# Optimization experiments

Hardware: AMD Instinct MI355X
Metric: run time of the kernel (lower is better)

Reference implementation:

```python
import jax, jax.numpy as jnp
import numpy as np

B, H, T, K, V = 4, 16, 2048, 128, 128


def setup_inputs() -> dict:
    key = jax.random.key(0)
    ks = jax.random.split(key, 5)
    q = jax.random.normal(ks[0], (B, H, T, K), dtype=jnp.float32)
    k = jax.random.normal(ks[1], (B, H, T, K), dtype=jnp.float32)
    v = jax.random.normal(ks[2], (B, H, T, V), dtype=jnp.float32)
    # g is a per-step log decay gate: small negative so exp(g) in (0.95, 1]
    g = -jax.random.uniform(ks[3], (B, H, T), dtype=jnp.float32) * 0.05
    # beta is the delta-rule step size, in (0, 1)
    beta = jax.random.uniform(ks[4], (B, H, T), dtype=jnp.float32)
    initial_state = jnp.zeros((B, H, K, V), dtype=jnp.float32)
    return {"q": q, "k": k, "v": v, "g": g, "beta": beta,
            "initial_state": initial_state}


def _l2norm(x, eps=1e-12):
    # matches F.normalize(p=2, dim=-1): x / max(||x||_2, eps)
    n = jnp.sqrt(jnp.sum(x * x, axis=-1, keepdims=True))
    return x / jnp.maximum(n, eps)


def reference(q, k, v, g, beta, initial_state):
    q = _l2norm(q)
    k = _l2norm(k)
    scale = q.shape[-1] ** -0.5  # default scale of chunk_gated_delta_rule

    # time-major for scan: [T, B, H, ...]
    qT = jnp.moveaxis(q, 2, 0) * scale
    kT = jnp.moveaxis(k, 2, 0)
    vT = jnp.moveaxis(v, 2, 0)
    gT = jnp.moveaxis(g, 2, 0)
    bT = jnp.moveaxis(beta, 2, 0)

    def step(S, inp):
        qt, kt, vt, gt, bt = inp  # qt/kt: [B,H,K], vt: [B,H,V], gt/bt: [B,H]
        S = S * jnp.exp(gt)[..., None, None]           # gated decay of state
        kS = jnp.einsum('bhk,bhkv->bhv', kt, S)        # current prediction
        dv = bt[..., None] * (vt - kS)                 # delta-rule correction
        S = S + jnp.einsum('bhk,bhv->bhkv', kt, dv)    # rank-1 state update
        ot = jnp.einsum('bhk,bhkv->bhv', qt, S)        # readout
        return S, ot

    final_state, oT = jax.lax.scan(step, initial_state, (qT, kT, vT, gT, bT))
    o = jnp.moveaxis(oT, 0, 2)  # [B,H,T,V]
    return o, final_state
```

## Files before the change

kernel.cpp:

```cpp
#include <hip/hip_runtime.h>
#include <math.h>

typedef float f32x16 __attribute__((ext_vector_type(16)));
typedef short s16x8 __attribute__((ext_vector_type(8)));
typedef unsigned int u32;

namespace {
constexpr int B_ = 4, H_ = 16, T_ = 2048, K_ = 128, V_ = 128;
constexpr int BHn = B_ * H_;
constexpr int C = 32;
constexpr int NCH = T_ / C;
constexpr int NS = 4;
constexpr int VS = V_ / NS;
constexpr float SCALE = 0.08838834764831845f;
constexpr int SK = 136;
constexpr int SRT = 36;
constexpr int SRU = 36;
constexpr int SG = 48;
constexpr int SF = 36;
constexpr size_t WSCH = 4608;
}

__device__ __forceinline__ ushort f2bf(float x) {
  unsigned u = __builtin_bit_cast(unsigned, x);
  u += 0x7FFF + ((u >> 16) & 1);
  return (ushort)(u >> 16);
}
__device__ __forceinline__ u32 cvtpk(float lo, float hi) {
  u32 r;
  asm("v_cvt_pk_bf16_f32 %0, %1, %2" : "=v"(r) : "v"(lo), "v"(hi));
  return r;
}
__device__ __forceinline__ int rowmap(int i, int lh) { return (i & 3) + 8 * (i >> 2) + 4 * lh; }

__device__ __forceinline__ void bar_lds() {
  asm volatile("s_waitcnt lgkmcnt(0)" ::: "memory");
  __builtin_amdgcn_s_barrier();
  asm volatile("" ::: "memory");
}

__device__ __forceinline__ s16x8 ld8u(const ushort* p) {
  uint2 a = *(const uint2*)(p);
  uint2 b = *(const uint2*)(p + 4);
  int4 r = make_int4((int)a.x, (int)a.y, (int)b.x, (int)b.y);
  return __builtin_bit_cast(s16x8, r);
}

__device__ __forceinline__ void packq(const f32x16& a, u32* u) {
  #pragma unroll
  for (int j = 0; j < 4; ++j) {
    u[2*j]   = cvtpk(a[4*j],   a[4*j+1]);
    u[2*j+1] = cvtpk(a[4*j+2], a[4*j+3]);
  }
}
__device__ __forceinline__ void swapfr(const u32* u, s16x8& f0, s16x8& f1) {
  u32 a0 = u[0], b0 = u[2], a1 = u[1], b1 = u[3];
  u32 a2 = u[4], b2 = u[6], a3 = u[5], b3 = u[7];
  asm("v_permlane32_swap_b32 %0, %1" : "+v"(a0), "+v"(b0));
  asm("v_permlane32_swap_b32 %0, %1" : "+v"(a1), "+v"(b1));
  asm("v_permlane32_swap_b32 %0, %1" : "+v"(a2), "+v"(b2));
  asm("v_permlane32_swap_b32 %0, %1" : "+v"(a3), "+v"(b3));
  f0 = __builtin_bit_cast(s16x8, make_int4((int)a0, (int)a1, (int)b0, (int)b1));
  f1 = __builtin_bit_cast(s16x8, make_int4((int)a2, (int)a3, (int)b2, (int)b3));
}

__device__ __forceinline__ f32x16 mm8(const ushort* A, const ushort* B, int lr, int lh) {
  f32x16 a0, a1;
  #pragma unroll
  for (int i = 0; i < 16; ++i) { a0[i] = 0.f; a1[i] = 0.f; }
  #pragma unroll
  for (int kb = 0; kb < 8; kb += 2) {
    const int o0 = lr * SK + 16 * kb + 8 * lh, o1 = o0 + 16;
    a0 = __builtin_amdgcn_mfma_f32_32x32x16_bf16(*(const s16x8*)(A + o0),
                                                 *(const s16x8*)(B + o0), a0, 0, 0, 0);
    a1 = __builtin_amdgcn_mfma_f32_32x32x16_bf16(*(const s16x8*)(A + o1),
                                                 *(const s16x8*)(B + o1), a1, 0, 0, 0);
  }
  return a0 + a1;
}

__global__ __launch_bounds__(256, 2)
void gdn_pre_kernel(const float* __restrict__ qg, const float* __restrict__ kg,
                    const float* __restrict__ gg, const float* __restrict__ bg,
                    char* __restrict__ ws)
{
  const int bid = blockIdx.x;
  const int bh = bid >> 6, ch = bid & 63;
  const int t = threadIdx.x, w = t >> 6, l = t & 63, lr = l & 31, lh = l >> 5;
  const int r8 = t >> 3, c8 = t & 7;
  const int t0 = ch * C;

  __shared__ __align__(16) ushort Kh[C * SK], Qh[C * SK];
  __shared__ __align__(16) float Mm[C * SF];
  __shared__ __align__(16) ushort Tt[C * 32], Gt[C * 32];
  __shared__ float ls_g[C], ls_b[C], ls_eb[C], ls_emb[C], ls_nq[C];

  {
    const float4* q4 = (const float4*)(qg + ((size_t)bh * T_ + t0 + r8) * K_);
    const float4* k4 = (const float4*)(kg + ((size_t)bh * T_ + t0 + r8) * K_);
    float4 qv[4], kv[4]; float sq = 0.f, sk = 0.f;
    #pragma unroll
    for (int c = 0; c < 4; ++c) {
      qv[c] = q4[c8 + 8 * c]; kv[c] = k4[c8 + 8 * c];
      sq += qv[c].x*qv[c].x + qv[c].y*qv[c].y + qv[c].z*qv[c].z + qv[c].w*qv[c].w;
      sk += kv[c].x*kv[c].x + kv[c].y*kv[c].y + kv[c].z*kv[c].z + kv[c].w*kv[c].w;
    }
    sq += __shfl_xor(sq, 1); sq += __shfl_xor(sq, 2); sq += __shfl_xor(sq, 4);
    sk += __shfl_xor(sk, 1); sk += __shfl_xor(sk, 2); sk += __shfl_xor(sk, 4);
    const float niq = SCALE / fmaxf(sqrtf(sq), 1e-12f);
    const float nik = 1.0f / fmaxf(sqrtf(sk), 1e-12f);
    if (c8 == 0) ls_nq[r8] = niq;
    #pragma unroll
    for (int c = 0; c < 4; ++c) {
      const int f4 = c8 + 8 * c;
      uint2 upk, upq;
      upk.x = cvtpk(kv[c].x * nik, kv[c].y * nik);
      upk.y = cvtpk(kv[c].z * nik, kv[c].w * nik);
      upq.x = cvtpk(qv[c].x * niq, qv[c].y * niq);
      upq.y = cvtpk(qv[c].z * niq, qv[c].w * niq);
      *(uint2*)(Kh + r8 * SK + f4 * 4) = upk;
      *(uint2*)(Qh + r8 * SK + f4 * 4) = upq;
    }
    if (t < C)          ls_g[t]     = gg[(size_t)bh * T_ + t0 + t];
    else if (t < 2 * C) ls_b[t - C] = bg[(size_t)bh * T_ + t0 + t - C];
  }
  __syncthreads();
  if (w == 3 && l < 32) {
    float x = ls_g[l];
    #pragma unroll
    for (int d = 1; d < 32; d <<= 1) { float y = __shfl_up(x, d); if (l >= d) x += y; }
    ls_eb[l] = expf(x); ls_emb[l] = expf(-x);
  }
  if (w == 0) {
    f32x16 acc = mm8(Kh, Kh, lr, lh);
    #pragma unroll
    for (int i = 0; i < 16; ++i) Mm[rowmap(i, lh) * SF + lr] = acc[i];
  }
  if (w == 1) {
    f32x16 acc = mm8(Qh, Kh, lr, lh);
    #pragma unroll
    for (int i = 0; i < 16; ++i) {
      int row = rowmap(i, lh);
      Gt[row * 32 + lr] = (lr <= row) ? f2bf(acc[i]) : (ushort)0;
    }
  }
  __syncthreads();
  if (w == 2 && l < 32) {
    const int j = l;
    float x[32];
    #pragma unroll
    for (int m = 0; m < 32; ++m) x[m] = (m == j) ? 1.f : 0.f;
    #pragma unroll
    for (int r = 1; r < 32; ++r) {
      const float* mr = Mm + r * SF;
      float p0 = 0.f, p1 = 0.f, p2 = 0.f, p3 = 0.f;
      #pragma unroll
      for (int jb = 0; jb + 4 <= r; jb += 4) {
        float4 m4 = *(const float4*)(mr + jb);
        p0 = fmaf(m4.x, x[jb + 0], p0);
        p1 = fmaf(m4.y, x[jb + 1], p1);
        p2 = fmaf(m4.z, x[jb + 2], p2);
        p3 = fmaf(m4.w, x[jb + 3], p3);
      }
      #pragma unroll
      for (int m = (r & ~3); m < r; ++m) p1 = fmaf(mr[m], x[m], p1);
      float xr = -ls_b[r] * ((p0 + p1) + (p2 + p3));
      if (r > j) x[r] = xr;
    }
    #pragma unroll
    for (int r = 0; r < 32; ++r) Tt[r * 32 + j] = f2bf(x[r]);
  }
  __syncthreads();
  {
    char* wsb = ws + ((size_t)bh * NCH + ch) * WSCH;
    u32* wT = (u32*)wsb; u32* wG = (u32*)(wsb + 2048); float* wS = (float*)(wsb + 4096);
    const u32* sT = (const u32*)Tt; const u32* sG = (const u32*)Gt;
    wT[t] = sT[t]; wT[t + 256] = sT[t + 256];
    wG[t] = sG[t]; wG[t + 256] = sG[t + 256];
    if (t < 32)      wS[t] = ls_eb[t];
    else if (t < 96) {
      int j = t - 32, r = j >> 1;
      wS[t] = (j & 1) ? ls_b[r] : ls_b[r] * ls_emb[r];
    } else if (t < 128) wS[t] = ls_nq[t - 96];
  }
}

__global__ __launch_bounds__(256, 1)
void gdn_seq_kernel(const float* __restrict__ qg, const float* __restrict__ kg,
                    const float* __restrict__ vg, const float* __restrict__ s0,
                    const char* __restrict__ ws, float* __restrict__ out)
{
  const int bid = blockIdx.x;
  const int xcd = bid & 7, qd = bid >> 3;
  const int bh = (qd >> 2) * 8 + xcd;
  const int v0 = (qd & 3) * VS;
  const int t = threadIdx.x, w = t >> 6, l = t & 63, lr = l & 31, lh = l >> 5;
  const int ts = t & 127;
  const int r4 = ts >> 2, c4 = ts & 3;

  __shared__ __align__(16) ushort Kh[2][C * SK];
  __shared__ __align__(16) ushort KhT[2][K_ * SRT];
  __shared__ __align__(16) ushort Tl[2][C * SG], Gl[3][C * SG];
  __shared__ __align__(16) float  vl[2][C * VS];
  __shared__ __align__(16) float  ls_eb[3][C];
  __shared__ __align__(16) float  ls_bbf[2][2 * C];
  __shared__ __align__(16) ushort UT[2][32 * SRU];
  __shared__ __align__(16) ushort SbT[2][32 * SK];

  const float* qh = qg + (size_t)bh * T_ * K_;
  const float* kh = kg + (size_t)bh * T_ * K_;
  const float* vh = vg + (size_t)bh * T_ * V_;
  const char* wsh = ws + (size_t)bh * NCH * WSCH;
  float* oh = out + (size_t)bh * T_ * V_;

  f32x16 Sst[4];
  s16x8 Sfrag[8];
  if (w == 0) {
    #pragma unroll
    for (int q = 0; q < 4; ++q) {
      const float* sp = s0 + ((size_t)bh * K_ + 32 * q) * V_ + v0 + lr;
      #pragma unroll
      for (int i = 0; i < 16; i += 2) {
        int row = rowmap(i, lh);
        Sst[q][i]     = sp[(size_t)row * V_];
        Sst[q][i + 1] = sp[(size_t)(row + 1) * V_];
      }
      u32 us[8]; packq(Sst[q], us);
      #pragma unroll
      for (int p = 0; p < 8; ++p)
        *(u32*)(&SbT[0][0] + lr * SK + 32 * q + rowmap(2 * p, lh)) = us[p];
      swapfr(us, Sfrag[2 * q], Sfrag[2 * q + 1]);
    }
  }

  float4 pq4[16]; float pniq = 0.f;
  auto qprefetch = [&](int cc) {
    const float4* q4 = (const float4*)(qh + (size_t)(cc * C + lr) * K_);
    #pragma unroll
    for (int kb = 0; kb < 8; ++kb) {
      pq4[2 * kb]     = q4[4 * kb + 2 * lh];
      pq4[2 * kb + 1] = q4[4 * kb + 2 * lh + 1];
    }
    pniq = ((const float*)(wsh + (size_t)cc * WSCH + 4096))[96 + lr];
  };

  float4 pk[8], pv[2];
  u32 pT[4], pG[4]; float psc = 0.f;
  auto prefetch = [&](int cc) {
    const float4* k4 = (const float4*)(kh + (size_t)(cc * C + r4) * K_);
    #pragma unroll
    for (int j = 0; j < 8; ++j) pk[j] = k4[c4 + 4 * j];
    const float4* v4 = (const float4*)(vh + (size_t)(cc * C + r4) * V_ + v0);
    pv[0] = v4[c4]; pv[1] = v4[c4 + 4];
    const char* wsb = wsh + (size_t)cc * WSCH;
    #pragma unroll
    for (int j = 0; j < 4; ++j) {
      pT[j] = ((const u32*)wsb)[ts + 128 * j];
      pG[j] = ((const u32*)(wsb + 2048))[ts + 128 * j];
    }
    psc = (ts < 96) ? ((const float*)(wsb + 4096))[ts] : 0.f;
  };
  auto stage = [&](int b, int b3) {
    float sk = 0.f;
    #pragma unroll
    for (int j = 0; j < 8; ++j)
      sk += pk[j].x*pk[j].x + pk[j].y*pk[j].y + pk[j].z*pk[j].z + pk[j].w*pk[j].w;
    sk += __shfl_xor(sk, 1); sk += __shfl_xor(sk, 2);
    const float nik = 1.0f / fmaxf(sqrtf(sk), 1e-12f);
    #pragma unroll
    for (int j = 0; j < 8; ++j) {
      const int f4 = c4 + 4 * j;
      uint2 upk;
      upk.x = cvtpk(pk[j].x * nik, pk[j].y * nik);
      upk.y = cvtpk(pk[j].z * nik, pk[j].w * nik);
      *(uint2*)(&Kh[b][0] + r4 * SK + 4 * f4) = upk;
      ushort* kt = &KhT[b][0] + (4 * f4) * SRT + r4;
      kt[0]       = (ushort)upk.x;
      kt[SRT]     = (ushort)(upk.x >> 16);
      kt[2 * SRT] = (ushort)upk.y;
      kt[3 * SRT] = (ushort)(upk.y >> 16);
    }
    *(float4*)(&vl[b][0] + r4 * VS + 4 * c4) = pv[0];
    *(float4*)(&vl[b][0] + r4 * VS + 4 * (c4 + 4)) = pv[1];
    #pragma unroll
    for (int j = 0; j < 4; ++j) {
      int e = ts + 128 * j;
      *(u32*)(&Tl[b][0]  + (e >> 4) * SG + 2 * (e & 15)) = pT[j];
      *(u32*)(&Gl[b3][0] + (e >> 4) * SG + 2 * (e & 15)) = pG[j];
    }
    if (ts < 32)      ls_eb[b3][ts]      = psc;
    else if (ts < 96) ls_bbf[b][ts - 32] = psc;
  };

  if (w >= 2)      { prefetch(0); stage(0, 0); prefetch(1); }
  else if (w == 1) { qprefetch(0); }
  bar_lds();

  f32x16 Xprev;
  for (int ch = 0; ch < NCH; ++ch) {
    const int cur = ch & 1, nxt = cur ^ 1, c3 = ch % 3;
    if (w == 0) {
      f32x16 a0, a1;
      #pragma unroll
      for (int i = 0; i < 16; ++i) { a0[i] = 0.f; a1[i] = 0.f; }
      #pragma unroll
      for (int kb = 0; kb < 8; kb += 2) {
        s16x8 ka = *(const s16x8*)(&Kh[cur][0] + lr * SK + 16 * kb + 8 * lh);
        s16x8 kbv = *(const s16x8*)(&Kh[cur][0] + lr * SK + 16 * (kb + 1) + 8 * lh);
        a0 = __builtin_amdgcn_mfma_f32_32x32x16_bf16(ka, Sfrag[kb], a0, 0, 0, 0);
        a1 = __builtin_amdgcn_mfma_f32_32x32x16_bf16(kbv, Sfrag[kb + 1], a1, 0, 0, 0);
      }
      f32x16 Wacc = a0 + a1;
      f32x16 Bv;
      #pragma unroll
      for (int i = 0; i < 16; ++i) {
        int row = rowmap(i, lh);
        float2 bb = ((const float2*)ls_bbf[cur])[row];
        Bv[i] = bb.x * vl[cur][row * VS + lr] - bb.y * Wacc[i];
      }
      u32 ub[8]; packq(Bv, ub);
      s16x8 bf0, bf1; swapfr(ub, bf0, bf1);
      f32x16 Uacc;
      #pragma unroll
      for (int i = 0; i < 16; ++i) Uacc[i] = 0.f;
      {
        s16x8 t0f = *(const s16x8*)(&Tl[cur][0] + lr * SG + 8 * lh);
        s16x8 t1f = *(const s16x8*)(&Tl[cur][0] + lr * SG + 16 + 8 * lh);
        Uacc = __builtin_amdgcn_mfma_f32_32x32x16_bf16(t0f, bf0, Uacc, 0, 0, 0);
        Uacc = __builtin_amdgcn_mfma_f32_32x32x16_bf16(t1f, bf1, Uacc, 0, 0, 0);
      }
      u32 uu[8]; packq(Uacc, uu);
      #pragma unroll
      for (int p = 0; p < 8; ++p)
        *(u32*)(&UT[cur][0] + lr * SRU + rowmap(2 * p, lh)) = uu[p];
      s16x8 uf0, uf1; swapfr(uu, uf0, uf1);
      const float ebL = ls_eb[c3][31];
      #pragma unroll
      for (int q = 0; q < 4; ++q) {
        f32x16 acc = Sst[q];
        s16x8 ka0 = ld8u(&KhT[cur][0] + (32 * q + lr) * SRT + 8 * lh);
        s16x8 ka1 = ld8u(&KhT[cur][0] + (32 * q + lr) * SRT + 16 + 8 * lh);
        acc = __builtin_amdgcn_mfma_f32_32x32x16_bf16(ka0, uf0, acc, 0, 0, 0);
        acc = __builtin_amdgcn_mfma_f32_32x32x16_bf16(ka1, uf1, acc, 0, 0, 0);
        #pragma unroll
        for (int i = 0; i < 16; ++i) Sst[q][i] = ebL * acc[i];
        u32 us[8]; packq(Sst[q], us);
        #pragma unroll
        for (int p = 0; p < 8; ++p)
          *(u32*)(&SbT[nxt][0] + lr * SK + 32 * q + rowmap(2 * p, lh)) = us[p];
        swapfr(us, Sfrag[2 * q], Sfrag[2 * q + 1]);
      }
    } else if (w == 1) {
      f32x16 x0, x1;
      #pragma unroll
      for (int i = 0; i < 16; ++i) { x0[i] = 0.f; x1[i] = 0.f; }
      #pragma unroll
      for (int kb = 0; kb < 8; kb += 2) {
        u32 qa0 = cvtpk(pq4[2*kb].x * pniq,   pq4[2*kb].y * pniq);
        u32 qa1 = cvtpk(pq4[2*kb].z * pniq,   pq4[2*kb].w * pniq);
        u32 qa2 = cvtpk(pq4[2*kb+1].x * pniq, pq4[2*kb+1].y * pniq);
        u32 qa3 = cvtpk(pq4[2*kb+1].z * pniq, pq4[2*kb+1].w * pniq);
        s16x8 qa = __builtin_bit_cast(s16x8, make_int4((int)qa0,(int)qa1,(int)qa2,(int)qa3));
        u32 qb0 = cvtpk(pq4[2*kb+2].x * pniq, pq4[2*kb+2].y * pniq);
        u32 qb1 = cvtpk(pq4[2*kb+2].z * pniq, pq4[2*kb+2].w * pniq);
        u32 qb2 = cvtpk(pq4[2*kb+3].x * pniq, pq4[2*kb+3].y * pniq);
        u32 qb3 = cvtpk(pq4[2*kb+3].z * pniq, pq4[2*kb+3].w * pniq);
        s16x8 qb = __builtin_bit_cast(s16x8, make_int4((int)qb0,(int)qb1,(int)qb2,(int)qb3));
        x0 = __builtin_amdgcn_mfma_f32_32x32x16_bf16(
                 qa, *(const s16x8*)(&SbT[cur][0] + lr * SK + 16 * kb + 8 * lh), x0, 0, 0, 0);
        x1 = __builtin_amdgcn_mfma_f32_32x32x16_bf16(
                 qb, *(const s16x8*)(&SbT[cur][0] + lr * SK + 16 * (kb + 1) + 8 * lh), x1, 0, 0, 0);
      }
      f32x16 Xn = x0 + x1;
      if (ch > 0) {
        const int pc = (ch - 1) & 1, p3 = (ch - 1) % 3, tp = (ch - 1) * C;
        f32x16 Oacc = Xprev;
        #pragma unroll
        for (int kb = 0; kb < 2; ++kb) {
          s16x8 a = *(const s16x8*)(&Gl[p3][0] + lr * SG + 16 * kb + 8 * lh);
          s16x8 b = ld8u(&UT[pc][0] + lr * SRU + 16 * kb + 8 * lh);
          Oacc = __builtin_amdgcn_mfma_f32_32x32x16_bf16(a, b, Oacc, 0, 0, 0);
        }
        #pragma unroll
        for (int i = 0; i < 16; ++i) {
          const int row = rowmap(i, lh);
          oh[(size_t)(tp + row) * V_ + v0 + lr] = ls_eb[p3][row] * Oacc[i];
        }
      }
      Xprev = Xn;
      if (ch + 1 < NCH) qprefetch(ch + 1);
    } else {
      if (ch + 1 < NCH) stage(nxt, (ch + 1) % 3);
      if (ch + 2 < NCH) prefetch(ch + 2);
    }
    bar_lds();
  }

  if (w == 1) {
    const int pc = (NCH - 1) & 1, p3 = (NCH - 1) % 3, tp = (NCH - 1) * C;
    f32x16 Oacc = Xprev;
    #pragma unroll
    for (int kb = 0; kb < 2; ++kb) {
      s16x8 a = *(const s16x8*)(&Gl[p3][0] + lr * SG + 16 * kb + 8 * lh);
      s16x8 b = ld8u(&UT[pc][0] + lr * SRU + 16 * kb + 8 * lh);
      Oacc = __builtin_amdgcn_mfma_f32_32x32x16_bf16(a, b, Oacc, 0, 0, 0);
    }
    #pragma unroll
    for (int i = 0; i < 16; ++i) {
      const int row = rowmap(i, lh);
      oh[(size_t)(tp + row) * V_ + v0 + lr] = ls_eb[p3][row] * Oacc[i];
    }
  }
  if (w == 0) {
    #pragma unroll
    for (int q = 0; q < 4; ++q) {
      float* sp = out + (size_t)BHn * T_ * V_
                      + ((size_t)bh * K_ + 32 * q) * V_ + v0 + lr;
      #pragma unroll
      for (int i = 0; i < 16; ++i)
        sp[(size_t)rowmap(i, lh) * V_] = Sst[q][i];
    }
  }
}

extern "C" void kernel_launch(void* const* d_in, const int* in_sizes, int n_in,
                              void* d_out, int out_size, void* d_ws, size_t ws_size,
                              hipStream_t stream) {
  const float* q    = (const float*)d_in[0];
  const float* k    = (const float*)d_in[1];
  const float* v    = (const float*)d_in[2];
  const float* g    = (const float*)d_in[3];
  const float* beta = (const float*)d_in[4];
  const float* s0   = (const float*)d_in[5];
  float* out = (float*)d_out;
  char* ws = (char*)d_ws;
  hipLaunchKernelGGL(gdn_pre_kernel, dim3(BHn * NCH), dim3(256), 0, stream,
                     q, k, g, beta, ws);
  hipLaunchKernelGGL(gdn_seq_kernel, dim3(BHn * NS), dim3(256), 0, stream,
                     q, k, v, s0, ws, out);
}
```

Baseline: 182.3 us.

## Load V, T and G fragments directly into registers, bypassing LDS staging

V, T and G tiles are no longer staged through shared memory by the producer warps. The warps that use them now prefetch them one chunk ahead straight into registers, with the loop unrolled by two to ping-pong the register buffers. The W and X MFMA chains are split into four independent accumulators for more ILP, the KhT fragment loads are hoisted ahead of the MFMAs, and the pre kernel's launch bound rises to three blocks per CU. This removes LDS traffic and bank pressure from the critical sequential warp, but adds register pressure and strided uncoalesced global loads on the compute warps.

```diff
diff --git a/kernel.cpp b/kernel.cpp
--- a/kernel.cpp
+++ b/kernel.cpp
@@ -16,7 +16,6 @@
 constexpr int SK = 136;
 constexpr int SRT = 36;
 constexpr int SRU = 36;
-constexpr int SG = 48;
 constexpr int SF = 36;
 constexpr size_t WSCH = 4608;
 }
@@ -79,7 +78,7 @@
   return a0 + a1;
 }
 
-__global__ __launch_bounds__(256, 2)
+__global__ __launch_bounds__(256, 3)
 void gdn_pre_kernel(const float* __restrict__ qg, const float* __restrict__ kg,
                     const float* __restrict__ gg, const float* __restrict__ bg,
                     char* __restrict__ ws)
@@ -200,8 +199,6 @@
 
   __shared__ __align__(16) ushort Kh[2][C * SK];
   __shared__ __align__(16) ushort KhT[2][K_ * SRT];
-  __shared__ __align__(16) ushort Tl[2][C * SG], Gl[3][C * SG];
-  __shared__ __align__(16) float  vl[2][C * VS];
   __shared__ __align__(16) float  ls_eb[3][C];
   __shared__ __align__(16) float  ls_bbf[2][2 * C];
   __shared__ __align__(16) ushort UT[2][32 * SRU];
@@ -215,6 +212,8 @@
 
   f32x16 Sst[4];
   s16x8 Sfrag[8];
+  float pvvA[16], pvvB[16];
+  s16x8 pTfA[2], pTfB[2];
   if (w == 0) {
     #pragma unroll
     for (int q = 0; q < 4; ++q) {
@@ -231,9 +230,19 @@
         *(u32*)(&SbT[0][0] + lr * SK + 32 * q + rowmap(2 * p, lh)) = us[p];
       swapfr(us, Sfrag[2 * q], Sfrag[2 * q + 1]);
     }
+    {
+      const float* vb = vh + (size_t)v0 + lr;
+      #pragma unroll
+      for (int i = 0; i < 16; ++i) pvvA[i] = vb[(size_t)rowmap(i, lh) * V_];
+      const ushort* Tg = (const ushort*)wsh;
+      pTfA[0] = *(const s16x8*)(Tg + lr * 32 + 8 * lh);
+      pTfA[1] = *(const s16x8*)(Tg + lr * 32 + 16 + 8 * lh);
+    }
   }
 
   float4 pq4[16]; float pniq = 0.f;
+  s16x8 pGf[2];
+  f32x16 Xprev;
   auto qprefetch = [&](int cc) {
     const float4* q4 = (const float4*)(qh + (size_t)(cc * C + lr) * K_);
     #pragma unroll
@@ -244,21 +253,12 @@
     pniq = ((const float*)(wsh + (size_t)cc * WSCH + 4096))[96 + lr];
   };
 
-  float4 pk[8], pv[2];
-  u32 pT[4], pG[4]; float psc = 0.f;
+  float4 pk[8]; float psc = 0.f;
   auto prefetch = [&](int cc) {
     const float4* k4 = (const float4*)(kh + (size_t)(cc * C + r4) * K_);
     #pragma unroll
     for (int j = 0; j < 8; ++j) pk[j] = k4[c4 + 4 * j];
-    const float4* v4 = (const float4*)(vh + (size_t)(cc * C + r4) * V_ + v0);
-    pv[0] = v4[c4]; pv[1] = v4[c4 + 4];
-    const char* wsb = wsh + (size_t)cc * WSCH;
-    #pragma unroll
-    for (int j = 0; j < 4; ++j) {
-      pT[j] = ((const u32*)wsb)[ts + 128 * j];
-      pG[j] = ((const u32*)(wsb + 2048))[ts + 128 * j];
-    }
-    psc = (ts < 96) ? ((const float*)(wsb + 4096))[ts] : 0.f;
+    psc = (ts < 96) ? ((const float*)(wsh + (size_t)cc * WSCH + 4096))[ts] : 0.f;
   };
   auto stage = [&](int b, int b3) {
     float sk = 0.f;
@@ -280,14 +280,6 @@
       kt[2 * SRT] = (ushort)upk.y;
       kt[3 * SRT] = (ushort)(upk.y >> 16);
     }
-    *(float4*)(&vl[b][0] + r4 * VS + 4 * c4) = pv[0];
-    *(float4*)(&vl[b][0] + r4 * VS + 4 * (c4 + 4)) = pv[1];
-    #pragma unroll
-    for (int j = 0; j < 4; ++j) {
-      int e = ts + 128 * j;
-      *(u32*)(&Tl[b][0]  + (e >> 4) * SG + 2 * (e & 15)) = pT[j];
-      *(u32*)(&Gl[b3][0] + (e >> 4) * SG + 2 * (e & 15)) = pG[j];
-    }
     if (ts < 32)      ls_eb[b3][ts]      = psc;
     else if (ts < 96) ls_bbf[b][ts - 32] = psc;
   };
@@ -296,39 +288,57 @@
   else if (w == 1) { qprefetch(0); }
   bar_lds();
 
-  f32x16 Xprev;
-  for (int ch = 0; ch < NCH; ++ch) {
-    const int cur = ch & 1, nxt = cur ^ 1, c3 = ch % 3;
+  #define MFMA __builtin_amdgcn_mfma_f32_32x32x16_bf16
+  auto iter = [&](int ch, int cur, float* pvvC, float* pvvN, s16x8* pTfC, s16x8* pTfN) {
+    const int nxt = cur ^ 1, c3 = ch % 3;
     if (w == 0) {
-      f32x16 a0, a1;
-      #pragma unroll
-      for (int i = 0; i < 16; ++i) { a0[i] = 0.f; a1[i] = 0.f; }
-      #pragma unroll
-      for (int kb = 0; kb < 8; kb += 2) {
-        s16x8 ka = *(const s16x8*)(&Kh[cur][0] + lr * SK + 16 * kb + 8 * lh);
-        s16x8 kbv = *(const s16x8*)(&Kh[cur][0] + lr * SK + 16 * (kb + 1) + 8 * lh);
-        a0 = __builtin_amdgcn_mfma_f32_32x32x16_bf16(ka, Sfrag[kb], a0, 0, 0, 0);
-        a1 = __builtin_amdgcn_mfma_f32_32x32x16_bf16(kbv, Sfrag[kb + 1], a1, 0, 0, 0);
-      }
-      f32x16 Wacc = a0 + a1;
+      if (ch + 1 < NCH) {
+        const float* vb = vh + (size_t)((ch + 1) * C) * V_ + v0 + lr;
+        #pragma unroll
+        for (int i = 0; i < 16; ++i) pvvN[i] = vb[(size_t)rowmap(i, lh) * V_];
+        const ushort* Tg = (const ushort*)(wsh + (size_t)(ch + 1) * WSCH);
+        pTfN[0] = *(const s16x8*)(Tg + lr * 32 + 8 * lh);
+        pTfN[1] = *(const s16x8*)(Tg + lr * 32 + 16 + 8 * lh);
+      }
+      s16x8 kt2[8];
+      #pragma unroll
+      for (int q = 0; q < 4; ++q) {
+        kt2[2*q]   = ld8u(&KhT[cur][0] + (32 * q + lr) * SRT + 8 * lh);
+        kt2[2*q+1] = ld8u(&KhT[cur][0] + (32 * q + lr) * SRT + 16 + 8 * lh);
+      }
+      float2 bbp[16];
+      #pragma unroll
+      for (int p = 0; p < 8; ++p) {
+        int row = rowmap(2 * p, lh);
+        bbp[2*p]   = ((const float2*)ls_bbf[cur])[row];
+        bbp[2*p+1] = ((const float2*)ls_bbf[cur])[row + 1];
+      }
+      float tv[16];
+      #pragma unroll
+      for (int i = 0; i < 16; ++i) tv[i] = bbp[i].x * pvvC[i];
+      f32x16 wa0, wa1, wa2, wa3;
+      #pragma unroll
+      for (int i = 0; i < 16; ++i) { wa0[i]=0.f; wa1[i]=0.f; wa2[i]=0.f; wa3[i]=0.f; }
+      const ushort* khc = &Kh[cur][0] + lr * SK + 8 * lh;
+      wa0 = MFMA(*(const s16x8*)(khc +   0), Sfrag[0], wa0, 0, 0, 0);
+      wa1 = MFMA(*(const s16x8*)(khc +  16), Sfrag[1], wa1, 0, 0, 0);
+      wa2 = MFMA(*(const s16x8*)(khc +  32), Sfrag[2], wa2, 0, 0, 0);
+      wa3 = MFMA(*(const s16x8*)(khc +  48), Sfrag[3], wa3, 0, 0, 0);
+      wa0 = MFMA(*(const s16x8*)(khc +  64), Sfrag[4], wa0, 0, 0, 0);
+      wa1 = MFMA(*(const s16x8*)(khc +  80), Sfrag[5], wa1, 0, 0, 0);
+      wa2 = MFMA(*(const s16x8*)(khc +  96), Sfrag[6], wa2, 0, 0, 0);
+      wa3 = MFMA(*(const s16x8*)(khc + 112), Sfrag[7], wa3, 0, 0, 0);
+      f32x16 Wacc = (wa0 + wa1) + (wa2 + wa3);
       f32x16 Bv;
       #pragma unroll
-      for (int i = 0; i < 16; ++i) {
-        int row = rowmap(i, lh);
-        float2 bb = ((const float2*)ls_bbf[cur])[row];
-        Bv[i] = bb.x * vl[cur][row * VS + lr] - bb.y * Wacc[i];
-      }
+      for (int i = 0; i < 16; ++i) Bv[i] = tv[i] - bbp[i].y * Wacc[i];
       u32 ub[8]; packq(Bv, ub);
       s16x8 bf0, bf1; swapfr(ub, bf0, bf1);
       f32x16 Uacc;
       #pragma unroll
       for (int i = 0; i < 16; ++i) Uacc[i] = 0.f;
-      {
-        s16x8 t0f = *(const s16x8*)(&Tl[cur][0] + lr * SG + 8 * lh);
-        s16x8 t1f = *(const s16x8*)(&Tl[cur][0] + lr * SG + 16 + 8 * lh);
-        Uacc = __builtin_amdgcn_mfma_f32_32x32x16_bf16(t0f, bf0, Uacc, 0, 0, 0);
-        Uacc = __builtin_amdgcn_mfma_f32_32x32x16_bf16(t1f, bf1, Uacc, 0, 0, 0);
-      }
+      Uacc = MFMA(pTfC[0], bf0, Uacc, 0, 0, 0);
+      Uacc = MFMA(pTfC[1], bf1, Uacc, 0, 0, 0);
       u32 uu[8]; packq(Uacc, uu);
       #pragma unroll
       for (int p = 0; p < 8; ++p)
@@ -338,10 +348,8 @@
       #pragma unroll
       for (int q = 0; q < 4; ++q) {
         f32x16 acc = Sst[q];
-        s16x8 ka0 = ld8u(&KhT[cur][0] + (32 * q + lr) * SRT + 8 * lh);
-        s16x8 ka1 = ld8u(&KhT[cur][0] + (32 * q + lr) * SRT + 16 + 8 * lh);
-        acc = __builtin_amdgcn_mfma_f32_32x32x16_bf16(ka0, uf0, acc, 0, 0, 0);
-        acc = __builtin_amdgcn_mfma_f32_32x32x16_bf16(ka1, uf1, acc, 0, 0, 0);
+        acc = MFMA(kt2[2*q],   uf0, acc, 0, 0, 0);
+        acc = MFMA(kt2[2*q+1], uf1, acc, 0, 0, 0);
         #pragma unroll
         for (int i = 0; i < 16; ++i) Sst[q][i] = ebL * acc[i];
         u32 us[8]; packq(Sst[q], us);
@@ -351,36 +359,30 @@
         swapfr(us, Sfrag[2 * q], Sfrag[2 * q + 1]);
       }
     } else if (w == 1) {
-      f32x16 x0, x1;
-      #pragma unroll
-      for (int i = 0; i < 16; ++i) { x0[i] = 0.f; x1[i] = 0.f; }
-      #pragma unroll
-      for (int kb = 0; kb < 8; kb += 2) {
-        u32 qa0 = cvtpk(pq4[2*kb].x * pniq,   pq4[2*kb].y * pniq);
-        u32 qa1 = cvtpk(pq4[2*kb].z * pniq,   pq4[2*kb].w * pniq);
-        u32 qa2 = cvtpk(pq4[2*kb+1].x * pniq, pq4[2*kb+1].y * pniq);
-        u32 qa3 = cvtpk(pq4[2*kb+1].z * pniq, pq4[2*kb+1].w * pniq);
-        s16x8 qa = __builtin_bit_cast(s16x8, make_int4((int)qa0,(int)qa1,(int)qa2,(int)qa3));
-        u32 qb0 = cvtpk(pq4[2*kb+2].x * pniq, pq4[2*kb+2].y * pniq);
-        u32 qb1 = cvtpk(pq4[2*kb+2].z * pniq, pq4[2*kb+2].w * pniq);
-        u32 qb2 = cvtpk(pq4[2*kb+3].x * pniq, pq4[2*kb+3].y * pniq);
-        u32 qb3 = cvtpk(pq4[2*kb+3].z * pniq, pq4[2*kb+3].w * pniq);
-        s16x8 qb = __builtin_bit_cast(s16x8, make_int4((int)qb0,(int)qb1,(int)qb2,(int)qb3));
-        x0 = __builtin_amdgcn_mfma_f32_32x32x16_bf16(
-                 qa, *(const s16x8*)(&SbT[cur][0] + lr * SK + 16 * kb + 8 * lh), x0, 0, 0, 0);
-        x1 = __builtin_amdgcn_mfma_f32_32x32x16_bf16(
-                 qb, *(const s16x8*)(&SbT[cur][0] + lr * SK + 16 * (kb + 1) + 8 * lh), x1, 0, 0, 0);
-      }
-      f32x16 Xn = x0 + x1;
+      f32x16 x0, x1, x2, x3;
+      #pragma unroll
+      for (int i = 0; i < 16; ++i) { x0[i]=0.f; x1[i]=0.f; x2[i]=0.f; x3[i]=0.f; }
+      #pragma unroll
+      for (int kb = 0; kb < 8; ++kb) {
+        u32 ca = cvtpk(pq4[2*kb].x * pniq,   pq4[2*kb].y * pniq);
+        u32 cb = cvtpk(pq4[2*kb].z * pniq,   pq4[2*kb].w * pniq);
+        u32 cc2 = cvtpk(pq4[2*kb+1].x * pniq, pq4[2*kb+1].y * pniq);
+        u32 cd = cvtpk(pq4[2*kb+1].z * pniq, pq4[2*kb+1].w * pniq);
+        s16x8 qa = __builtin_bit_cast(s16x8, make_int4((int)ca,(int)cb,(int)cc2,(int)cd));
+        s16x8 sb = *(const s16x8*)(&SbT[cur][0] + lr * SK + 16 * kb + 8 * lh);
+        switch (kb & 3) {
+          case 0: x0 = MFMA(qa, sb, x0, 0, 0, 0); break;
+          case 1: x1 = MFMA(qa, sb, x1, 0, 0, 0); break;
+          case 2: x2 = MFMA(qa, sb, x2, 0, 0, 0); break;
+          default: x3 = MFMA(qa, sb, x3, 0, 0, 0); break;
+        }
+      }
+      f32x16 Xn = (x0 + x1) + (x2 + x3);
       if (ch > 0) {
-        const int pc = (ch - 1) & 1, p3 = (ch - 1) % 3, tp = (ch - 1) * C;
+        const int pc = nxt, p3 = (ch - 1) % 3, tp = (ch - 1) * C;
         f32x16 Oacc = Xprev;
-        #pragma unroll
-        for (int kb = 0; kb < 2; ++kb) {
-          s16x8 a = *(const s16x8*)(&Gl[p3][0] + lr * SG + 16 * kb + 8 * lh);
-          s16x8 b = ld8u(&UT[pc][0] + lr * SRU + 16 * kb + 8 * lh);
-          Oacc = __builtin_amdgcn_mfma_f32_32x32x16_bf16(a, b, Oacc, 0, 0, 0);
-        }
+        Oacc = MFMA(pGf[0], ld8u(&UT[pc][0] + lr * SRU + 8 * lh),      Oacc, 0, 0, 0);
+        Oacc = MFMA(pGf[1], ld8u(&UT[pc][0] + lr * SRU + 16 + 8 * lh), Oacc, 0, 0, 0);
         #pragma unroll
         for (int i = 0; i < 16; ++i) {
           const int row = rowmap(i, lh);
@@ -388,23 +390,32 @@
         }
       }
       Xprev = Xn;
+      {
+        const ushort* Gg = (const ushort*)(wsh + (size_t)ch * WSCH + 2048);
+        pGf[0] = *(const s16x8*)(Gg + lr * 32 + 8 * lh);
+        pGf[1] = *(const s16x8*)(Gg + lr * 32 + 16 + 8 * lh);
+      }
       if (ch + 1 < NCH) qprefetch(ch + 1);
     } else {
       if (ch + 1 < NCH) stage(nxt, (ch + 1) % 3);
       if (ch + 2 < NCH) prefetch(ch + 2);
     }
     bar_lds();
-  }
+  };
+
+  for (int ch = 0; ch < NCH; ch += 2) {
+    iter(ch,     0, pvvA, pvvB, pTfA, pTfB);
+    iter(ch + 1, 1, pvvB, pvvA, pTfB, pTfA);
+  }
+  #undef MFMA
 
   if (w == 1) {
     const int pc = (NCH - 1) & 1, p3 = (NCH - 1) % 3, tp = (NCH - 1) * C;
     f32x16 Oacc = Xprev;
-    #pragma unroll
-    for (int kb = 0; kb < 2; ++kb) {
-      s16x8 a = *(const s16x8*)(&Gl[p3][0] + lr * SG + 16 * kb + 8 * lh);
-      s16x8 b = ld8u(&UT[pc][0] + lr * SRU + 16 * kb + 8 * lh);
-      Oacc = __builtin_amdgcn_mfma_f32_32x32x16_bf16(a, b, Oacc, 0, 0, 0);
-    }
+    Oacc = __builtin_amdgcn_mfma_f32_32x32x16_bf16(
+        pGf[0], ld8u(&UT[pc][0] + lr * SRU + 8 * lh), Oacc, 0, 0, 0);
+    Oacc = __builtin_amdgcn_mfma_f32_32x32x16_bf16(
+        pGf[1], ld8u(&UT[pc][0] + lr * SRU + 16 + 8 * lh), Oacc, 0, 0, 0);
     #pragma unroll
     for (int i = 0; i < 16; ++i) {
       const int row = rowmap(i, lh);
```

Result: faster. 154.5 us (-15.2%).
